# Kernel tuning notes

Measured on AMD Instinct MI355X. Metric: run time of the kernel, lower is better.

## Reference

```python
import jax, jax.numpy as jnp
import numpy as np

N_HARMONIC = 6
CONCAT = (3,)  # cfg.append_distance: concat embedding after this layer index
N_LAYERS = 8


def harmonic_embedding(x):
    # x: [N, 3] -> [N, 6*2*3 + 3] = [N, 39]
    freqs = 2.0 ** jnp.arange(N_HARMONIC, dtype=x.dtype)  # omega0 = 1.0, logspace
    embed = (x[..., None] * freqs).reshape(*x.shape[:-1], -1)  # [N, 18]
    return jnp.concatenate([jnp.sin(embed), jnp.cos(embed), x], axis=-1)


def setup_inputs() -> dict:
    key = jax.random.key(0)
    N, H, E = 262144, 256, 39
    ks = jax.random.split(key, 11)
    inp = {"points": jax.random.normal(ks[0], (N, 3), dtype=jnp.float32)}
    in_dims = [E, H, H, H, E + H, H, H, H]  # skip-concat before layer 4
    for i, d_in in enumerate(in_dims):
        scale = 1.0 / np.sqrt(d_in)
        inp[f"w{i}"] = jax.random.normal(ks[i + 1], (d_in, H), dtype=jnp.float32) * scale
        inp[f"b{i}"] = jnp.zeros((H,), dtype=jnp.float32)
    inp["wsdf"] = jax.random.normal(ks[9], (H, 1), dtype=jnp.float32) * (1.0 / np.sqrt(H))
    inp["bsdf"] = jnp.zeros((1,), dtype=jnp.float32)
    return inp


def reference(points, w0, b0, w1, b1, w2, b2, w3, b3, w4, b4, w5, b5, w6, b6, w7, b7, wsdf, bsdf):
    ws = [w0, w1, w2, w3, w4, w5, w6, w7]
    bs = [b0, b1, b2, b3, b4, b5, b6, b7]
    emb = harmonic_embedding(points.reshape(-1, 3))  # [N, 39]
    x = emb
    for i in range(N_LAYERS):
        x = jax.nn.relu(x @ ws[i] + bs[i])
        if i in CONCAT:
            x = jnp.concatenate([emb, x], axis=-1)  # torch.cat([add, xyz])
    return x @ wsdf + bsdf  # [N, 1] signed distance
```

## Files before the change

kernel.cpp:

```cpp
#include <hip/hip_runtime.h>
#include <hip/hip_fp16.h>

typedef _Float16 f16x8 __attribute__((ext_vector_type(8)));
typedef _Float16 f16x4 __attribute__((ext_vector_type(4)));
typedef _Float16 f16x2 __attribute__((ext_vector_type(2)));
typedef float    f32x16 __attribute__((ext_vector_type(16)));
typedef float    f32x4 __attribute__((ext_vector_type(4)));

#define SH 264
#define SE 56

struct LayerPtrs {
  const float* w[8];
  const float* b[8];
};

__global__ void prep_weights(LayerPtrs P, f16x8* __restrict__ wf) {
  int gid = blockIdx.x * 256 + threadIdx.x;
  if (gid >= 60416) return;
  const int OFF[9] = {0,1536,9728,17920,26112,35840,44032,52224,60416};
  int l = 0;
  while (gid >= OFF[l+1]) ++l;
  int f = gid - OFF[l];
  int lane = f & 63;
  int t = f >> 6;
  int mtile = t & 7;
  int kc = t >> 3;
  int col = mtile * 32 + (lane & 31);
  int kb  = (lane >> 5) * 8;
  const float* w = P.w[l];
  f16x8 v;
#pragma unroll
  for (int j = 0; j < 8; ++j) {
    float x = 0.f;
    if (l == 4) {
      if (kc < 3) {
        int k = kc * 16 + kb + j;
        if (k < 39) x = w[k * 256 + col];
      } else {
        int k = (kc - 3) * 16 + kb + j;
        x = w[(39 + k) * 256 + col];
      }
    } else if (l == 0) {
      int k = kc * 16 + kb + j;
      if (k < 39) x = w[k * 256 + col];
    } else {
      int k = kc * 16 + kb + j;
      x = w[k * 256 + col];
    }
    v[j] = (_Float16)x;
  }
  wf[gid] = v;
}

#define MFMA __builtin_amdgcn_mfma_f32_32x32x16_f16

__device__ __forceinline__ void aload2(f16x8& d0, f16x8& d1, const f16x8* p) {
  asm volatile("global_load_dwordx4 %0, %2, off\n\t"
               "global_load_dwordx4 %1, %2, off offset:1024"
               : "=&v"(d0), "=&v"(d1)
               : "v"(p));
}

__device__ __forceinline__ void mfma8(f16x8 a0, f16x8 a1,
                                      f16x8 v0, f16x8 v1, f16x8 v2, f16x8 v3,
                                      f32x16 acc[2][4]) {
  acc[0][0] = MFMA(a0, v0, acc[0][0], 0, 0, 0);
  acc[0][1] = MFMA(a0, v1, acc[0][1], 0, 0, 0);
  acc[0][2] = MFMA(a0, v2, acc[0][2], 0, 0, 0);
  acc[0][3] = MFMA(a0, v3, acc[0][3], 0, 0, 0);
  acc[1][0] = MFMA(a1, v0, acc[1][0], 0, 0, 0);
  acc[1][1] = MFMA(a1, v1, acc[1][1], 0, 0, 0);
  acc[1][2] = MFMA(a1, v2, acc[1][2], 0, 0, 0);
  acc[1][3] = MFMA(a1, v3, acc[1][3], 0, 0, 0);
}

__device__ __forceinline__ void mfma8_z(f16x8 a0, f16x8 a1,
                                        f16x8 v0, f16x8 v1, f16x8 v2, f16x8 v3,
                                        f32x16 acc[2][4]) {
  const f32x16 z = {};
  acc[0][0] = MFMA(a0, v0, z, 0, 0, 0);
  acc[0][1] = MFMA(a0, v1, z, 0, 0, 0);
  acc[0][2] = MFMA(a0, v2, z, 0, 0, 0);
  acc[0][3] = MFMA(a0, v3, z, 0, 0, 0);
  acc[1][0] = MFMA(a1, v0, z, 0, 0, 0);
  acc[1][1] = MFMA(a1, v1, z, 0, 0, 0);
  acc[1][2] = MFMA(a1, v2, z, 0, 0, 0);
  acc[1][3] = MFMA(a1, v3, z, 0, 0, 0);
}

template<int NKC, bool FIRST, int RSTRIDE>
__device__ __forceinline__ void mm(const f16x8* __restrict__ wb,
                                   const char* __restrict__ r0,
                                   f32x16 acc[2][4]) {
  f16x8 a00, a01, a10, a11;
  aload2(a00, a01, wb);
  if (NKC > 1) aload2(a10, a11, wb + 512);
  f16x8 v0 = *(const f16x8*)(r0);
  f16x8 v1 = *(const f16x8*)(r0 + RSTRIDE);
  f16x8 v2 = *(const f16x8*)(r0 + 2 * RSTRIDE);
  f16x8 v3 = *(const f16x8*)(r0 + 3 * RSTRIDE);
#pragma unroll
  for (int kc = 0; kc < NKC; ++kc) {
    f16x8 na0, na1, nv0, nv1, nv2, nv3;
    if (kc + 2 < NKC) aload2(na0, na1, wb + (kc + 2) * 512);
    if (kc + 1 < NKC) {
      const char* rp = r0 + 32 * (kc + 1);
      nv0 = *(const f16x8*)(rp);
      nv1 = *(const f16x8*)(rp + RSTRIDE);
      nv2 = *(const f16x8*)(rp + 2 * RSTRIDE);
      nv3 = *(const f16x8*)(rp + 3 * RSTRIDE);
    }
    if (kc + 2 < NKC)      asm volatile("s_waitcnt vmcnt(4)");
    else if (kc + 1 < NKC) asm volatile("s_waitcnt vmcnt(2)");
    else                   asm volatile("s_waitcnt vmcnt(0)");
    __builtin_amdgcn_sched_barrier(0);
    if (FIRST && kc == 0) mfma8_z(a00, a01, v0, v1, v2, v3, acc);
    else                  mfma8 (a00, a01, v0, v1, v2, v3, acc);
    if (kc + 1 < NKC) {
      a00 = a10; a01 = a11;
      v0 = nv0; v1 = nv1; v2 = nv2; v3 = nv3;
    }
    if (kc + 2 < NKC) { a10 = na0; a11 = na1; }
  }
}

__device__ __forceinline__ f16x4 relu_cvt4(float a0, float a1, float a2, float a3) {
  f16x2 lo = __builtin_bit_cast(f16x2, __builtin_amdgcn_cvt_pkrtz(a0, a1));
  f16x2 hi = __builtin_bit_cast(f16x2, __builtin_amdgcn_cvt_pkrtz(a2, a3));
  union { f16x4 v; f16x2 h[2]; } u;
  u.h[0] = lo; u.h[1] = hi;
  f16x4 z = {};
  return __builtin_elementwise_max(u.v, z);
}

__device__ __forceinline__ void store_epi(f32x16 acc[2][4],
                                          const float* __restrict__ bias,
                                          int wg, int p0, int h,
                                          _Float16* __restrict__ Hs) {
#pragma unroll
  for (int mt = 0; mt < 2; ++mt) {
    int hb = wg * 64 + mt * 32 + 4 * h;
#pragma unroll
    for (int g = 0; g < 4; ++g) {
      f32x4 q = *(const f32x4*)&bias[hb + 8 * g];
#pragma unroll
      for (int nt = 0; nt < 4; ++nt) {
        f16x4 o = relu_cvt4(acc[mt][nt][4 * g + 0] + q[0],
                            acc[mt][nt][4 * g + 1] + q[1],
                            acc[mt][nt][4 * g + 2] + q[2],
                            acc[mt][nt][4 * g + 3] + q[3]);
        *(f16x4*)&Hs[(nt * 32 + p0) * SH + hb + 8 * g] = o;
      }
    }
  }
}

__device__ __forceinline__ void emb_channel(_Float16* __restrict__ Erow,
                                            int c, float x) {
  _Float16 sv[6], cv[6];
  float fr = 1.f;
#pragma unroll
  for (int k = 0; k < 6; ++k) {
    float e = x * fr;
    sv[k] = (_Float16)__sinf(e);
    cv[k] = (_Float16)__cosf(e);
    fr *= 2.f;
  }
#pragma unroll
  for (int k = 0; k < 6; k += 2) {
    f16x2 s2 = {sv[k], sv[k + 1]};
    f16x2 c2 = {cv[k], cv[k + 1]};
    *(f16x2*)&Erow[6 * c + k]      = s2;
    *(f16x2*)&Erow[18 + 6 * c + k] = c2;
  }
  Erow[36 + c] = (_Float16)x;
}

__global__ __launch_bounds__(256, 2)
void mlp_fused(const float* __restrict__ points,
               LayerPtrs P,
               const f16x8* __restrict__ wf,
               const float* __restrict__ wsdf,
               const float* __restrict__ bsdf,
               float* __restrict__ out) {
  __shared__ __align__(16) _Float16 Hs[128 * SH];
  __shared__ __align__(16) _Float16 Es[128 * SE];
  const int tid = threadIdx.x;
  const int blk = blockIdx.x;

  const int lane = tid & 63;
  const int wg   = tid >> 6;
  const int p0   = lane & 31;
  const int h    = lane >> 5;

  const f16x8* wb = wf + wg * 128 + lane;

  {
    int p = tid & 127, part = tid >> 7;
    _Float16* Erow = &Es[p * SE];
    const float* pp = &points[(blk * 128 + p) * 3];
    if (part == 0) {
      emb_channel(Erow, 0, pp[0]);
      emb_channel(Erow, 1, pp[1]);
    } else {
      emb_channel(Erow, 2, pp[2]);
      Erow[39] = (_Float16)0.f;
      f16x4 z4 = {};
      *(f16x4*)&Erow[40] = z4;
      *(f16x4*)&Erow[44] = z4;
      *(f16x4*)&Erow[48] = z4;
      *(f16x4*)&Erow[52] = z4;
    }
  }
  __syncthreads();

  const char* hR = (const char*)Hs + (p0 * SH + 8 * h) * 2;
  const char* eR = (const char*)Es + (p0 * SE + 8 * h) * 2;

  f32x16 acc[2][4];

  mm<3, true, 32 * SE * 2>(wb, eR, acc);
  store_epi(acc, P.b[0], wg, p0, h, Hs);
  __syncthreads();

  const int WOFF[8] = {0, 1536, 9728, 17920, 26112, 35840, 44032, 52224};

#pragma unroll
  for (int l = 1; l < 4; ++l) {
    mm<16, true, 32 * SH * 2>(wb + WOFF[l], hR, acc);
    __syncthreads();
    store_epi(acc, P.b[l], wg, p0, h, Hs);
    __syncthreads();
  }

  {
    mm<3, true, 32 * SE * 2>(wb + 26112, eR, acc);
    mm<16, false, 32 * SH * 2>(wb + 27648, hR, acc);
    __syncthreads();
    store_epi(acc, P.b[4], wg, p0, h, Hs);
    __syncthreads();
  }

#pragma unroll
  for (int l = 5; l < 7; ++l) {
    mm<16, true, 32 * SH * 2>(wb + WOFF[l], hR, acc);
    __syncthreads();
    store_epi(acc, P.b[l], wg, p0, h, Hs);
    __syncthreads();
  }

  mm<16, true, 32 * SH * 2>(wb + 52224, hR, acc);
  {
    float part[4] = {0.f, 0.f, 0.f, 0.f};
    const float* b7 = P.b[7];
#pragma unroll
    for (int mt = 0; mt < 2; ++mt) {
#pragma unroll
      for (int g = 0; g < 4; ++g) {
        int idx = wg * 64 + mt * 32 + 8 * g + 4 * h;
        f32x4 qb = *(const f32x4*)&b7[idx];
        f32x4 qw = *(const f32x4*)&wsdf[idx];
#pragma unroll
        for (int nt = 0; nt < 4; ++nt)
#pragma unroll
          for (int r = 0; r < 4; ++r)
            part[nt] += fmaxf(acc[mt][nt][4 * g + r] + qb[r], 0.f) * qw[r];
      }
    }
    float* PB = (float*)Es;
#pragma unroll
    for (int nt = 0; nt < 4; ++nt)
      PB[(wg * 2 + h) * 128 + nt * 32 + p0] = part[nt];
    __syncthreads();
    if (tid < 128) {
      float s = bsdf[0];
#pragma unroll
      for (int j = 0; j < 8; ++j) s += PB[j * 128 + tid];
      out[blk * 128 + tid] = s;
    }
  }
}

extern "C" void kernel_launch(void* const* d_in, const int* in_sizes, int n_in,
                              void* d_out, int out_size, void* d_ws, size_t ws_size,
                              hipStream_t stream) {
  const float* points = (const float*)d_in[0];
  LayerPtrs P;
  for (int i = 0; i < 8; ++i) {
    P.w[i] = (const float*)d_in[1 + 2 * i];
    P.b[i] = (const float*)d_in[2 + 2 * i];
  }
  const float* wsdf = (const float*)d_in[17];
  const float* bsdf = (const float*)d_in[18];
  f16x8* wf = (f16x8*)d_ws;

  int N = in_sizes[0] / 3;
  prep_weights<<<236, 256, 0, stream>>>(P, wf);
  mlp_fused<<<N / 128, 256, 0, stream>>>(points, P, wf, wsdf, bsdf, (float*)d_out);
}
```

Measured before the change: 297.4 us.

## Prefetch next layer weights across barriers, fuse skip-layer K loop, raise MFMA priority

The first two weight chunks of the next layer are now loaded right after each layer's MMA loop, so the global load latency overlaps the barriers and the bias/ReLU epilogue instead of sitting at the start of the next matmul. The skip-concat layer is handled by one 19-chunk pipelined loop that reads from the embedding tile and then the hidden tile, replacing two separate loops and the pipeline drain between them. MFMA groups are wrapped in s_setprio to favour the wave issuing matrix work, and the bias add is done as a vector. This keeps four weight registers live across epilogues, which raises register pressure, and it relies on in-order vmcnt counting staying correct with the bias loads issued in between.

```diff
diff --git a/kernel.cpp b/kernel.cpp
--- a/kernel.cpp
+++ b/kernel.cpp
@@ -62,9 +62,19 @@
                : "v"(p));
 }
 
+struct APre { f16x8 a00, a01, a10, a11; };
+
+__device__ __forceinline__ APre apre(const f16x8* __restrict__ wb) {
+  APre p;
+  aload2(p.a00, p.a01, wb);
+  aload2(p.a10, p.a11, wb + 512);
+  return p;
+}
+
 __device__ __forceinline__ void mfma8(f16x8 a0, f16x8 a1,
                                       f16x8 v0, f16x8 v1, f16x8 v2, f16x8 v3,
                                       f32x16 acc[2][4]) {
+  __builtin_amdgcn_s_setprio(1);
   acc[0][0] = MFMA(a0, v0, acc[0][0], 0, 0, 0);
   acc[0][1] = MFMA(a0, v1, acc[0][1], 0, 0, 0);
   acc[0][2] = MFMA(a0, v2, acc[0][2], 0, 0, 0);
@@ -73,12 +83,14 @@
   acc[1][1] = MFMA(a1, v1, acc[1][1], 0, 0, 0);
   acc[1][2] = MFMA(a1, v2, acc[1][2], 0, 0, 0);
   acc[1][3] = MFMA(a1, v3, acc[1][3], 0, 0, 0);
+  __builtin_amdgcn_s_setprio(0);
 }
 
 __device__ __forceinline__ void mfma8_z(f16x8 a0, f16x8 a1,
                                         f16x8 v0, f16x8 v1, f16x8 v2, f16x8 v3,
                                         f32x16 acc[2][4]) {
   const f32x16 z = {};
+  __builtin_amdgcn_s_setprio(1);
   acc[0][0] = MFMA(a0, v0, z, 0, 0, 0);
   acc[0][1] = MFMA(a0, v1, z, 0, 0, 0);
   acc[0][2] = MFMA(a0, v2, z, 0, 0, 0);
@@ -87,15 +99,14 @@
   acc[1][1] = MFMA(a1, v1, z, 0, 0, 0);
   acc[1][2] = MFMA(a1, v2, z, 0, 0, 0);
   acc[1][3] = MFMA(a1, v3, z, 0, 0, 0);
+  __builtin_amdgcn_s_setprio(0);
 }
 
 template<int NKC, bool FIRST, int RSTRIDE>
 __device__ __forceinline__ void mm(const f16x8* __restrict__ wb,
                                    const char* __restrict__ r0,
-                                   f32x16 acc[2][4]) {
-  f16x8 a00, a01, a10, a11;
-  aload2(a00, a01, wb);
-  if (NKC > 1) aload2(a10, a11, wb + 512);
+                                   f32x16 acc[2][4], APre p) {
+  f16x8 a00 = p.a00, a01 = p.a01, a10 = p.a10, a11 = p.a11;
   f16x8 v0 = *(const f16x8*)(r0);
   f16x8 v1 = *(const f16x8*)(r0 + RSTRIDE);
   f16x8 v2 = *(const f16x8*)(r0 + 2 * RSTRIDE);
@@ -125,9 +136,53 @@
   }
 }
 
-__device__ __forceinline__ f16x4 relu_cvt4(float a0, float a1, float a2, float a3) {
-  f16x2 lo = __builtin_bit_cast(f16x2, __builtin_amdgcn_cvt_pkrtz(a0, a1));
-  f16x2 hi = __builtin_bit_cast(f16x2, __builtin_amdgcn_cvt_pkrtz(a2, a3));
+template<int RSE, int RSH>
+__device__ __forceinline__ void mm4(const f16x8* __restrict__ wb,
+                                    const char* __restrict__ eR,
+                                    const char* __restrict__ hR,
+                                    f32x16 acc[2][4], APre p) {
+  constexpr int NKC = 19;
+  f16x8 a00 = p.a00, a01 = p.a01, a10 = p.a10, a11 = p.a11;
+  f16x8 v0 = *(const f16x8*)(eR);
+  f16x8 v1 = *(const f16x8*)(eR + RSE);
+  f16x8 v2 = *(const f16x8*)(eR + 2 * RSE);
+  f16x8 v3 = *(const f16x8*)(eR + 3 * RSE);
+#pragma unroll
+  for (int kc = 0; kc < NKC; ++kc) {
+    f16x8 na0, na1, nv0, nv1, nv2, nv3;
+    if (kc + 2 < NKC) aload2(na0, na1, wb + (kc + 2) * 512);
+    if (kc + 1 < NKC) {
+      if (kc + 1 < 3) {
+        const char* rp = eR + 32 * (kc + 1);
+        nv0 = *(const f16x8*)(rp);
+        nv1 = *(const f16x8*)(rp + RSE);
+        nv2 = *(const f16x8*)(rp + 2 * RSE);
+        nv3 = *(const f16x8*)(rp + 3 * RSE);
+      } else {
+        const char* rp = hR + 32 * (kc + 1 - 3);
+        nv0 = *(const f16x8*)(rp);
+        nv1 = *(const f16x8*)(rp + RSH);
+        nv2 = *(const f16x8*)(rp + 2 * RSH);
+        nv3 = *(const f16x8*)(rp + 3 * RSH);
+      }
+    }
+    if (kc + 2 < NKC)      asm volatile("s_waitcnt vmcnt(4)");
+    else if (kc + 1 < NKC) asm volatile("s_waitcnt vmcnt(2)");
+    else                   asm volatile("s_waitcnt vmcnt(0)");
+    __builtin_amdgcn_sched_barrier(0);
+    if (kc == 0) mfma8_z(a00, a01, v0, v1, v2, v3, acc);
+    else         mfma8 (a00, a01, v0, v1, v2, v3, acc);
+    if (kc + 1 < NKC) {
+      a00 = a10; a01 = a11;
+      v0 = nv0; v1 = nv1; v2 = nv2; v3 = nv3;
+    }
+    if (kc + 2 < NKC) { a10 = na0; a11 = na1; }
+  }
+}
+
+__device__ __forceinline__ f16x4 relu_cvt4(f32x4 s) {
+  f16x2 lo = __builtin_bit_cast(f16x2, __builtin_amdgcn_cvt_pkrtz(s[0], s[1]));
+  f16x2 hi = __builtin_bit_cast(f16x2, __builtin_amdgcn_cvt_pkrtz(s[2], s[3]));
   union { f16x4 v; f16x2 h[2]; } u;
   u.h[0] = lo; u.h[1] = hi;
   f16x4 z = {};
@@ -146,11 +201,9 @@
       f32x4 q = *(const f32x4*)&bias[hb + 8 * g];
 #pragma unroll
       for (int nt = 0; nt < 4; ++nt) {
-        f16x4 o = relu_cvt4(acc[mt][nt][4 * g + 0] + q[0],
-                            acc[mt][nt][4 * g + 1] + q[1],
-                            acc[mt][nt][4 * g + 2] + q[2],
-                            acc[mt][nt][4 * g + 3] + q[3]);
-        *(f16x4*)&Hs[(nt * 32 + p0) * SH + hb + 8 * g] = o;
+        f32x4 s = {acc[mt][nt][4 * g + 0], acc[mt][nt][4 * g + 1],
+                   acc[mt][nt][4 * g + 2], acc[mt][nt][4 * g + 3]};
+        *(f16x4*)&Hs[(nt * 32 + p0) * SH + hb + 8 * g] = relu_cvt4(s + q);
       }
     }
   }
@@ -195,6 +248,9 @@
   const int h    = lane >> 5;
 
   const f16x8* wb = wf + wg * 128 + lane;
+  const int WOFF[8] = {0, 1536, 9728, 17920, 26112, 35840, 44032, 52224};
+
+  APre ap = apre(wb);
 
   {
     int p = tid & 127, part = tid >> 7;
@@ -220,23 +276,23 @@
 
   f32x16 acc[2][4];
 
-  mm<3, true, 32 * SE * 2>(wb, eR, acc);
+  mm<3, true, 32 * SE * 2>(wb, eR, acc, ap);
+  ap = apre(wb + WOFF[1]);
   store_epi(acc, P.b[0], wg, p0, h, Hs);
   __syncthreads();
 
-  const int WOFF[8] = {0, 1536, 9728, 17920, 26112, 35840, 44032, 52224};
-
 #pragma unroll
   for (int l = 1; l < 4; ++l) {
-    mm<16, true, 32 * SH * 2>(wb + WOFF[l], hR, acc);
+    mm<16, true, 32 * SH * 2>(wb + WOFF[l], hR, acc, ap);
+    ap = apre(wb + WOFF[l + 1]);
     __syncthreads();
     store_epi(acc, P.b[l], wg, p0, h, Hs);
     __syncthreads();
   }
 
   {
-    mm<3, true, 32 * SE * 2>(wb + 26112, eR, acc);
-    mm<16, false, 32 * SH * 2>(wb + 27648, hR, acc);
+    mm4<32 * SE * 2, 32 * SH * 2>(wb + 26112, eR, hR, acc, ap);
+    ap = apre(wb + WOFF[5]);
     __syncthreads();
     store_epi(acc, P.b[4], wg, p0, h, Hs);
     __syncthreads();
@@ -244,13 +300,14 @@
 
 #pragma unroll
   for (int l = 5; l < 7; ++l) {
-    mm<16, true, 32 * SH * 2>(wb + WOFF[l], hR, acc);
+    mm<16, true, 32 * SH * 2>(wb + WOFF[l], hR, acc, ap);
+    ap = apre(wb + WOFF[l + 1]);
     __syncthreads();
     store_epi(acc, P.b[l], wg, p0, h, Hs);
     __syncthreads();
   }
 
-  mm<16, true, 32 * SH * 2>(wb + 52224, hR, acc);
+  mm<16, true, 32 * SH * 2>(wb + 52224, hR, acc, ap);
   {
     float part[4] = {0.f, 0.f, 0.f, 0.f};
     const float* b7 = P.b[7];
```

Measured after the change: 298.0 us. No clear change (+0.2%).

## Halve points per block, double-buffer hidden activations, deepen weight prefetch

Applied to the files above, without the earlier changes.

Each block now processes 64 points instead of 128, halving per-wave accumulators and MFMA count per weight fragment. The hidden activation buffer is split into two ping-pong LDS buffers so each layer needs only one barrier instead of two. Weight prefetch depth increases from two to three k-chunks. The trade-off is that weights are reloaded from cache twice as often per point, lowering arithmetic intensity relative to weight traffic.

```diff
diff --git a/kernel.cpp b/kernel.cpp
--- a/kernel.cpp
+++ b/kernel.cpp
@@ -9,6 +9,7 @@
 
 #define SH 264
 #define SE 56
+#define PTS 64
 
 struct LayerPtrs {
   const float* w[8];
@@ -62,66 +63,54 @@
                : "v"(p));
 }
 
-__device__ __forceinline__ void mfma8(f16x8 a0, f16x8 a1,
-                                      f16x8 v0, f16x8 v1, f16x8 v2, f16x8 v3,
-                                      f32x16 acc[2][4]) {
+__device__ __forceinline__ void mfma4(f16x8 a0, f16x8 a1, f16x8 v0, f16x8 v1,
+                                      f32x16 acc[2][2]) {
   acc[0][0] = MFMA(a0, v0, acc[0][0], 0, 0, 0);
   acc[0][1] = MFMA(a0, v1, acc[0][1], 0, 0, 0);
-  acc[0][2] = MFMA(a0, v2, acc[0][2], 0, 0, 0);
-  acc[0][3] = MFMA(a0, v3, acc[0][3], 0, 0, 0);
   acc[1][0] = MFMA(a1, v0, acc[1][0], 0, 0, 0);
   acc[1][1] = MFMA(a1, v1, acc[1][1], 0, 0, 0);
-  acc[1][2] = MFMA(a1, v2, acc[1][2], 0, 0, 0);
-  acc[1][3] = MFMA(a1, v3, acc[1][3], 0, 0, 0);
-}
-
-__device__ __forceinline__ void mfma8_z(f16x8 a0, f16x8 a1,
-                                        f16x8 v0, f16x8 v1, f16x8 v2, f16x8 v3,
-                                        f32x16 acc[2][4]) {
+}
+
+__device__ __forceinline__ void mfma4_z(f16x8 a0, f16x8 a1, f16x8 v0, f16x8 v1,
+                                        f32x16 acc[2][2]) {
   const f32x16 z = {};
   acc[0][0] = MFMA(a0, v0, z, 0, 0, 0);
   acc[0][1] = MFMA(a0, v1, z, 0, 0, 0);
-  acc[0][2] = MFMA(a0, v2, z, 0, 0, 0);
-  acc[0][3] = MFMA(a0, v3, z, 0, 0, 0);
   acc[1][0] = MFMA(a1, v0, z, 0, 0, 0);
   acc[1][1] = MFMA(a1, v1, z, 0, 0, 0);
-  acc[1][2] = MFMA(a1, v2, z, 0, 0, 0);
-  acc[1][3] = MFMA(a1, v3, z, 0, 0, 0);
 }
 
 template<int NKC, bool FIRST, int RSTRIDE>
 __device__ __forceinline__ void mm(const f16x8* __restrict__ wb,
                                    const char* __restrict__ r0,
-                                   f32x16 acc[2][4]) {
-  f16x8 a00, a01, a10, a11;
+                                   f32x16 acc[2][2]) {
+  f16x8 a00, a01, b00, b01, c00, c01;
   aload2(a00, a01, wb);
-  if (NKC > 1) aload2(a10, a11, wb + 512);
+  if (NKC > 1) aload2(b00, b01, wb + 512);
+  if (NKC > 2) aload2(c00, c01, wb + 1024);
   f16x8 v0 = *(const f16x8*)(r0);
   f16x8 v1 = *(const f16x8*)(r0 + RSTRIDE);
-  f16x8 v2 = *(const f16x8*)(r0 + 2 * RSTRIDE);
-  f16x8 v3 = *(const f16x8*)(r0 + 3 * RSTRIDE);
 #pragma unroll
   for (int kc = 0; kc < NKC; ++kc) {
-    f16x8 na0, na1, nv0, nv1, nv2, nv3;
-    if (kc + 2 < NKC) aload2(na0, na1, wb + (kc + 2) * 512);
+    f16x8 na0, na1, nv0, nv1;
+    if (kc + 3 < NKC) aload2(na0, na1, wb + (kc + 3) * 512);
     if (kc + 1 < NKC) {
       const char* rp = r0 + 32 * (kc + 1);
       nv0 = *(const f16x8*)(rp);
       nv1 = *(const f16x8*)(rp + RSTRIDE);
-      nv2 = *(const f16x8*)(rp + 2 * RSTRIDE);
-      nv3 = *(const f16x8*)(rp + 3 * RSTRIDE);
-    }
-    if (kc + 2 < NKC)      asm volatile("s_waitcnt vmcnt(4)");
+    }
+    if (kc + 3 < NKC)      asm volatile("s_waitcnt vmcnt(6)");
+    else if (kc + 2 < NKC) asm volatile("s_waitcnt vmcnt(4)");
     else if (kc + 1 < NKC) asm volatile("s_waitcnt vmcnt(2)");
     else                   asm volatile("s_waitcnt vmcnt(0)");
     __builtin_amdgcn_sched_barrier(0);
-    if (FIRST && kc == 0) mfma8_z(a00, a01, v0, v1, v2, v3, acc);
-    else                  mfma8 (a00, a01, v0, v1, v2, v3, acc);
+    if (FIRST && kc == 0) mfma4_z(a00, a01, v0, v1, acc);
+    else                  mfma4 (a00, a01, v0, v1, acc);
     if (kc + 1 < NKC) {
-      a00 = a10; a01 = a11;
-      v0 = nv0; v1 = nv1; v2 = nv2; v3 = nv3;
-    }
-    if (kc + 2 < NKC) { a10 = na0; a11 = na1; }
+      a00 = b00; a01 = b01; b00 = c00; b01 = c01;
+      v0 = nv0; v1 = nv1;
+    }
+    if (kc + 3 < NKC) { c00 = na0; c01 = na1; }
   }
 }
 
@@ -134,10 +123,10 @@
   return __builtin_elementwise_max(u.v, z);
 }
 
-__device__ __forceinline__ void store_epi(f32x16 acc[2][4],
+__device__ __forceinline__ void store_epi(f32x16 acc[2][2],
                                           const float* __restrict__ bias,
                                           int wg, int p0, int h,
-                                          _Float16* __restrict__ Hs) {
+                                          _Float16* __restrict__ Hw) {
 #pragma unroll
   for (int mt = 0; mt < 2; ++mt) {
     int hb = wg * 64 + mt * 32 + 4 * h;
@@ -145,12 +134,12 @@
     for (int g = 0; g < 4; ++g) {
       f32x4 q = *(const f32x4*)&bias[hb + 8 * g];
 #pragma unroll
-      for (int nt = 0; nt < 4; ++nt) {
+      for (int nt = 0; nt < 2; ++nt) {
         f16x4 o = relu_cvt4(acc[mt][nt][4 * g + 0] + q[0],
                             acc[mt][nt][4 * g + 1] + q[1],
                             acc[mt][nt][4 * g + 2] + q[2],
                             acc[mt][nt][4 * g + 3] + q[3]);
-        *(f16x4*)&Hs[(nt * 32 + p0) * SH + hb + 8 * g] = o;
+        *(f16x4*)&Hw[(nt * 32 + p0) * SH + hb + 8 * g] = o;
       }
     }
   }
@@ -184,8 +173,9 @@
                const float* __restrict__ wsdf,
                const float* __restrict__ bsdf,
                float* __restrict__ out) {
-  __shared__ __align__(16) _Float16 Hs[128 * SH];
-  __shared__ __align__(16) _Float16 Es[128 * SE];
+  __shared__ __align__(16) _Float16 Hs0[PTS * SH];
+  __shared__ __align__(16) _Float16 Hs1[PTS * SH];
+  __shared__ __align__(16) _Float16 Es[PTS * SE];
   const int tid = threadIdx.x;
   const int blk = blockIdx.x;
 
@@ -197,14 +187,11 @@
   const f16x8* wb = wf + wg * 128 + lane;
 
   {
-    int p = tid & 127, part = tid >> 7;
+    int p = tid & 63, part = tid >> 6;
     _Float16* Erow = &Es[p * SE];
-    const float* pp = &points[(blk * 128 + p) * 3];
-    if (part == 0) {
-      emb_channel(Erow, 0, pp[0]);
-      emb_channel(Erow, 1, pp[1]);
+    if (part < 3) {
+      emb_channel(Erow, part, points[(blk * PTS + p) * 3 + part]);
     } else {
-      emb_channel(Erow, 2, pp[2]);
       Erow[39] = (_Float16)0.f;
       f16x4 z4 = {};
       *(f16x4*)&Erow[40] = z4;
@@ -215,44 +202,38 @@
   }
   __syncthreads();
 
-  const char* hR = (const char*)Hs + (p0 * SH + 8 * h) * 2;
-  const char* eR = (const char*)Es + (p0 * SE + 8 * h) * 2;
-
-  f32x16 acc[2][4];
+  const char* h0R = (const char*)Hs0 + (p0 * SH + 8 * h) * 2;
+  const char* h1R = (const char*)Hs1 + (p0 * SH + 8 * h) * 2;
+  const char* eR  = (const char*)Es  + (p0 * SE + 8 * h) * 2;
+
+  f32x16 acc[2][2];
+  const int WOFF[8] = {0, 1536, 9728, 17920, 26112, 35840, 44032, 52224};
 
   mm<3, true, 32 * SE * 2>(wb, eR, acc);
-  store_epi(acc, P.b[0], wg, p0, h, Hs);
-  __syncthreads();
-
-  const int WOFF[8] = {0, 1536, 9728, 17920, 26112, 35840, 44032, 52224};
-
-#pragma unroll
-  for (int l = 1; l < 4; ++l) {
-    mm<16, true, 32 * SH * 2>(wb + WOFF[l], hR, acc);
-    __syncthreads();
-    store_epi(acc, P.b[l], wg, p0, h, Hs);
-    __syncthreads();
-  }
-
+  store_epi(acc, P.b[0], wg, p0, h, Hs0);
+  __syncthreads();
+  mm<16, true, 32 * SH * 2>(wb + WOFF[1], h0R, acc);
+  store_epi(acc, P.b[1], wg, p0, h, Hs1);
+  __syncthreads();
+  mm<16, true, 32 * SH * 2>(wb + WOFF[2], h1R, acc);
+  store_epi(acc, P.b[2], wg, p0, h, Hs0);
+  __syncthreads();
+  mm<16, true, 32 * SH * 2>(wb + WOFF[3], h0R, acc);
+  store_epi(acc, P.b[3], wg, p0, h, Hs1);
+  __syncthreads();
+  mm<3, true, 32 * SE * 2>(wb + 26112, eR, acc);
+  mm<16, false, 32 * SH * 2>(wb + 27648, h1R, acc);
+  store_epi(acc, P.b[4], wg, p0, h, Hs0);
+  __syncthreads();
+  mm<16, true, 32 * SH * 2>(wb + WOFF[5], h0R, acc);
+  store_epi(acc, P.b[5], wg, p0, h, Hs1);
+  __syncthreads();
+  mm<16, true, 32 * SH * 2>(wb + WOFF[6], h1R, acc);
+  store_epi(acc, P.b[6], wg, p0, h, Hs0);
+  __syncthreads();
+  mm<16, true, 32 * SH * 2>(wb + WOFF[7], h0R, acc);
   {
-    mm<3, true, 32 * SE * 2>(wb + 26112, eR, acc);
-    mm<16, false, 32 * SH * 2>(wb + 27648, hR, acc);
-    __syncthreads();
-    store_epi(acc, P.b[4], wg, p0, h, Hs);
-    __syncthreads();
-  }
-
-#pragma unroll
-  for (int l = 5; l < 7; ++l) {
-    mm<16, true, 32 * SH * 2>(wb + WOFF[l], hR, acc);
-    __syncthreads();
-    store_epi(acc, P.b[l], wg, p0, h, Hs);
-    __syncthreads();
-  }
-
-  mm<16, true, 32 * SH * 2>(wb + 52224, hR, acc);
-  {
-    float part[4] = {0.f, 0.f, 0.f, 0.f};
+    float part0 = 0.f, part1 = 0.f;
     const float* b7 = P.b[7];
 #pragma unroll
     for (int mt = 0; mt < 2; ++mt) {
@@ -262,22 +243,21 @@
         f32x4 qb = *(const f32x4*)&b7[idx];
         f32x4 qw = *(const f32x4*)&wsdf[idx];
 #pragma unroll
-        for (int nt = 0; nt < 4; ++nt)
-#pragma unroll
-          for (int r = 0; r < 4; ++r)
-            part[nt] += fmaxf(acc[mt][nt][4 * g + r] + qb[r], 0.f) * qw[r];
+        for (int r = 0; r < 4; ++r) {
+          part0 += fmaxf(acc[mt][0][4 * g + r] + qb[r], 0.f) * qw[r];
+          part1 += fmaxf(acc[mt][1][4 * g + r] + qb[r], 0.f) * qw[r];
+        }
       }
     }
     float* PB = (float*)Es;
-#pragma unroll
-    for (int nt = 0; nt < 4; ++nt)
-      PB[(wg * 2 + h) * 128 + nt * 32 + p0] = part[nt];
+    PB[(wg * 2 + h) * 64 + p0]      = part0;
+    PB[(wg * 2 + h) * 64 + 32 + p0] = part1;
     __syncthreads();
-    if (tid < 128) {
+    if (tid < PTS) {
       float s = bsdf[0];
 #pragma unroll
-      for (int j = 0; j < 8; ++j) s += PB[j * 128 + tid];
-      out[blk * 128 + tid] = s;
+      for (int j = 0; j < 8; ++j) s += PB[j * 64 + tid];
+      out[blk * PTS + tid] = s;
     }
   }
 }
@@ -297,5 +277,5 @@
 
   int N = in_sizes[0] / 3;
   prep_weights<<<236, 256, 0, stream>>>(P, wf);
-  mlp_fused<<<N / 128, 256, 0, stream>>>(points, P, wf, wsdf, bsdf, (float*)d_out);
-}
+  mlp_fused<<<N / PTS, 256, 0, stream>>>(points, P, wf, wsdf, bsdf, (float*)d_out);
+}
```

Result: slower. 318.6 us (+7.1%).
